# Performance work log

Hardware: AMD Instinct MI355X
Metric: run time of the kernel (lower is better)

Reference implementation:

```python
import jax, jax.numpy as jnp
import numpy as np

B, S, D = 2, 2048, 2048
H, KVH, HD = 32, 8, 64  # n_heads, n_kv_heads, head_dim
REP = H // KVH


def setup_inputs() -> dict:
    key = jax.random.key(0)
    k0, k1, k2, k3, k4 = jax.random.split(key, 5)
    x = jax.random.normal(k0, (B, S, D), dtype=jnp.float32)
    # Linear weights stored as (in, out); matches torch nn.Linear(in,out).weight.T
    scale = 1.0 / np.sqrt(D)
    wq = jax.random.normal(k1, (D, H * HD), dtype=jnp.float32) * scale
    wk = jax.random.normal(k2, (D, KVH * HD), dtype=jnp.float32) * scale
    wv = jax.random.normal(k3, (D, KVH * HD), dtype=jnp.float32) * scale
    wo = jax.random.normal(k4, (H * HD, D), dtype=jnp.float32) * scale
    mask = jnp.tril(jnp.ones((S, S), dtype=bool))[None, None]  # [1,1,S,S] causal
    return {"x": x, "wq": wq, "wk": wk, "wv": wv, "wo": wo, "mask": mask}


def reference(x, wq, wk, wv, wo, mask):
    # Projections
    q = (x @ wq).reshape(B, S, KVH, REP, HD)   # Q head h = g*REP + r -> group g
    k = (x @ wk).reshape(B, S, KVH, HD)
    v = (x @ wv).reshape(B, S, KVH, HD)
    # Grouped attention: never materialize repeated K/V (same math as repeat_kv)
    scores = jnp.einsum('bqgrd,bkgd->bgrqk', q, k) / jnp.sqrt(jnp.asarray(HD, x.dtype))
    m = mask[:, :, None]  # [1,1,1,S,S] broadcasts over (group, rep)
    scores = jnp.where(m, scores, -jnp.inf)
    probs = jax.nn.softmax(scores, axis=-1)  # [B,KVH,REP,S,S]
    out = jnp.einsum('bgrqk,bkgd->bqgrd', probs, v)  # [B,S,KVH,REP,HD]
    out = out.reshape(B, S, H * HD)
    return out @ wo
```

## Files before the change

kernel.cpp:

```cpp
#include <hip/hip_runtime.h>
#include <stdint.h>

typedef __bf16 bf16x8 __attribute__((ext_vector_type(8)));
typedef float  f32x4  __attribute__((ext_vector_type(4)));
typedef float  f32x16 __attribute__((ext_vector_type(16)));

#define QSCALE 0.18033688011112042f

typedef __attribute__((address_space(1))) const void* as1cv;
typedef __attribute__((address_space(3))) void*       as3v;

__device__ __forceinline__ void gload16(const void* g, void* l) {
  __builtin_amdgcn_global_load_lds((as1cv)g, (as3v)l, 16, 0, 0);
}

__device__ __forceinline__ unsigned short f2b(float f) {
  union { float f; unsigned int u; } v; v.f = f;
  unsigned int r = v.u + 0x7fffu + ((v.u >> 16) & 1u);
  return (unsigned short)(r >> 16);
}

__device__ __forceinline__ float b2f(unsigned short s) {
  union { unsigned int u; float f; } v; v.u = (unsigned int)s << 16;
  return v.f;
}

#if __has_builtin(__builtin_amdgcn_exp2f)
__device__ __forceinline__ float fexp2(float x) { return __builtin_amdgcn_exp2f(x); }
#else
__device__ __forceinline__ float fexp2(float x) {
  float r;
  asm volatile("v_exp_f32 %0, %1\n\ts_nop 1" : "=v"(r) : "v"(x));
  return r;
}
#endif

__global__ void detect_dtype(const unsigned short* __restrict__ x, int* __restrict__ flag) {
  const int t = threadIdx.x;
  bool big = false;
  for (int i = t; i < 1024; i += 64) {
    float f = b2f(x[i]);
    if (!(fabsf(f) < 1e6f)) big = true;
  }
  if (t == 0) *flag = 0;
  __syncthreads();
  if (__any(big) && t == 0) *flag = 1;
}

__global__ __launch_bounds__(256) void convert_x(const void* __restrict__ src,
                                                 unsigned short* __restrict__ dst,
                                                 const int* __restrict__ flag) {
  const int i = blockIdx.x * 256 + threadIdx.x;
  if (*flag) {
    float4 a = ((const float4*)src)[2 * i];
    float4 b = ((const float4*)src)[2 * i + 1];
    union { unsigned short o[8]; uint4 v; } u;
    u.o[0] = f2b(a.x); u.o[1] = f2b(a.y); u.o[2] = f2b(a.z); u.o[3] = f2b(a.w);
    u.o[4] = f2b(b.x); u.o[5] = f2b(b.y); u.o[6] = f2b(b.z); u.o[7] = f2b(b.w);
    ((uint4*)dst)[i] = u.v;
  } else {
    ((uint4*)dst)[i] = ((const uint4*)src)[i];
  }
}

__global__ __launch_bounds__(256) void transpose_w(const void* __restrict__ src, int R, int C,
                                                   unsigned short* __restrict__ dst,
                                                   const int* __restrict__ flag) {
  __shared__ unsigned short tile[64][72];
  const int t = threadIdx.x;
  const int r = t >> 2;
  const int c0 = (t & 3) << 4;
  const int gr = blockIdx.y * 64 + r;
  const int gc = blockIdx.x * 64 + c0;
  if (*flag) {
    const float* s = (const float*)src + (size_t)gr * C + gc;
#pragma unroll
    for (int j = 0; j < 16; j += 4) {
      float4 v = *(const float4*)(s + j);
      tile[r][c0 + j + 0] = f2b(v.x);
      tile[r][c0 + j + 1] = f2b(v.y);
      tile[r][c0 + j + 2] = f2b(v.z);
      tile[r][c0 + j + 3] = f2b(v.w);
    }
  } else {
    const unsigned short* s = (const unsigned short*)src + (size_t)gr * C + gc;
    *(uint4*)&tile[r][c0]     = *(const uint4*)s;
    *(uint4*)&tile[r][c0 + 8] = *(const uint4*)(s + 8);
  }
  __syncthreads();
  const int c    = t >> 2;
  const int rblk = (t & 3) << 4;
  union { unsigned short o[16]; uint4 v[2]; } u;
#pragma unroll
  for (int j = 0; j < 16; ++j) u.o[j] = tile[rblk + j][c];
  unsigned short* d = dst + (size_t)(blockIdx.x * 64 + c) * R + blockIdx.y * 64 + rblk;
  *(uint4*)d       = u.v[0];
  *(uint4*)(d + 8) = u.v[1];
}

__global__ __launch_bounds__(256) void gemm_bt2(const unsigned short* __restrict__ A,
                                                const unsigned short* __restrict__ Bt,
                                                void* __restrict__ Cv,
                                                unsigned short* __restrict__ vtout,
                                                int M, int N, int K, int scale_cols,
                                                const int* __restrict__ f32flag) {
  __shared__ unsigned short As[2][128 * 64];
  __shared__ unsigned short Bs[2][128 * 64];
  const int t = threadIdx.x;
  const int lane = t & 63;
  const int wave = t >> 6;
  const int wm = wave >> 1, wn = wave & 1;
  int bx, by;
  {
    const int nx = (int)gridDim.x;
    const int nwg = nx * (int)gridDim.y;
    const int wg = (int)blockIdx.y * nx + (int)blockIdx.x;
    const int cpx = nwg >> 3;
    const int swz = (wg & 7) * cpx + (wg >> 3);
    bx = swz % nx; by = swz / nx;
  }
  const int m0 = by * 128, n0 = bx * 128;
  const int fr = lane & 15;
  const int kb = (lane >> 4) << 4;

  int rowS[4], dofS[4], scS[4];
#pragma unroll
  for (int i = 0; i < 4; ++i) {
    int off = i * 4096 + t * 16;
    dofS[i] = off;
    rowS[i] = off >> 7;
    scS[i]  = (off & 127) ^ ((rowS[i] & 7) << 4);
  }
  const char* pA[4];
  const char* pB[4];
#pragma unroll
  for (int i = 0; i < 4; ++i) {
    pA[i] = (const char*)(A  + (size_t)(m0 + rowS[i]) * K) + scS[i];
    pB[i] = (const char*)(Bt + (size_t)(n0 + rowS[i]) * K) + scS[i];
  }

  f32x4 acc[4][4] = {};
  const int NT = K >> 6;

#pragma unroll
  for (int i = 0; i < 4; ++i) {
    gload16(pA[i], (char*)As[0] + dofS[i]);
    gload16(pB[i], (char*)Bs[0] + dofS[i]);
  }
  __syncthreads();

  for (int kt = 0; kt < NT; ++kt) {
    if (kt + 1 < NT) {
      const int kby = (kt + 1) * 128;
      const int bsel = (kt + 1) & 1;
#pragma unroll
      for (int i = 0; i < 4; ++i) {
        gload16(pA[i] + kby, (char*)As[bsel] + dofS[i]);
        gload16(pB[i] + kby, (char*)Bs[bsel] + dofS[i]);
      }
    }
    const char* Ab = (const char*)As[kt & 1];
    const char* Bb = (const char*)Bs[kt & 1];
#pragma unroll
    for (int ks = 0; ks < 2; ++ks) {
      bf16x8 af[4], bfv[4];
#pragma unroll
      for (int i = 0; i < 4; ++i) {
        const int ra = wm * 64 + i * 16 + fr;
        af[i] = *(const bf16x8*)(Ab + ra * 128 + ((ks * 64 + kb) ^ ((ra & 7) << 4)));
        const int rb = wn * 64 + i * 16 + fr;
        bfv[i] = *(const bf16x8*)(Bb + rb * 128 + ((ks * 64 + kb) ^ ((rb & 7) << 4)));
      }
      __builtin_amdgcn_s_setprio(1);
#pragma unroll
      for (int i = 0; i < 4; ++i)
#pragma unroll
        for (int j = 0; j < 4; ++j)
          acc[i][j] = __builtin_amdgcn_mfma_f32_16x16x32_bf16(af[i], bfv[j], acc[i][j], 0, 0, 0);
      __builtin_amdgcn_s_setprio(0);
    }
    __syncthreads();
  }

  const int cm0 = m0 + wm * 64 + ((lane >> 4) << 2);
  const int cn0 = n0 + wn * 64 + fr;
  if (vtout && n0 >= 2560) {
    const int bb = m0 >> 11;
#pragma unroll
    for (int i = 0; i < 4; ++i) {
      const int s0 = cm0 + i * 16;
#pragma unroll
      for (int j = 0; j < 4; ++j) {
        const int d = cn0 + j * 16 - 2560;
        uint2 pr;
        pr.x = (unsigned int)f2b(acc[i][j][0]) | ((unsigned int)f2b(acc[i][j][1]) << 16);
        pr.y = (unsigned int)f2b(acc[i][j][2]) | ((unsigned int)f2b(acc[i][j][3]) << 16);
        *(uint2*)(vtout + (size_t)(bb * 512 + d) * 2048 + (s0 & 2047)) = pr;
      }
    }
    return;
  }
  const bool of32 = f32flag && (*f32flag != 0);
  if (of32) {
    float* C = (float*)Cv;
#pragma unroll
    for (int i = 0; i < 4; ++i)
#pragma unroll
      for (int j = 0; j < 4; ++j) {
        float sc = (cn0 + j * 16 < scale_cols) ? QSCALE : 1.0f;
#pragma unroll
        for (int r = 0; r < 4; ++r)
          C[(size_t)(cm0 + i * 16 + r) * N + (cn0 + j * 16)] = acc[i][j][r] * sc;
      }
  } else {
    unsigned short* C = (unsigned short*)Cv;
#pragma unroll
    for (int i = 0; i < 4; ++i)
#pragma unroll
      for (int j = 0; j < 4; ++j) {
        float sc = (cn0 + j * 16 < scale_cols) ? QSCALE : 1.0f;
#pragma unroll
        for (int r = 0; r < 4; ++r)
          C[(size_t)(cm0 + i * 16 + r) * N + (cn0 + j * 16)] = f2b(acc[i][j][r] * sc);
      }
  }
}

__global__ __launch_bounds__(256) void attn_fwd6(const unsigned short* __restrict__ qkv,
                                                 const unsigned short* __restrict__ vt,
                                                 unsigned short* __restrict__ ob) {
  __shared__ unsigned short Ks[2][64 * 64];
  __shared__ unsigned short Vs[2][64 * 64];
  const int t = threadIdx.x, lane = t & 63, w = t >> 6;
  const int half = lane >> 5, q32 = lane & 31;
  const int g = blockIdx.y, b = blockIdx.z;
  const int h = g * 4 + w;
  const size_t bS = (size_t)b * 2048;
  const size_t vtb = ((size_t)((b << 3) + g)) * 64;

  int rowS[2], dofS[2], cbS[2];
#pragma unroll
  for (int i = 0; i < 2; ++i) {
    int off = i * 4096 + t * 16;
    dofS[i] = off;
    rowS[i] = off >> 7;
    cbS[i]  = (off & 127) ^ ((rowS[i] & 7) << 4);
  }

  for (int ph = 0; ph < 2; ++ph) {
    const int qt32 = ph ? 63 - (int)blockIdx.x : (int)blockIdx.x;
    const int nkt = (qt32 >> 1) + 1;
    const int q_glob = qt32 * 32 + q32;
    if (ph) __syncthreads();

    bf16x8 qf[4];
    {
      const unsigned short* qrow = qkv + (bS + q_glob) * 3072 + h * 64 + half * 8;
#pragma unroll
      for (int c = 0; c < 4; ++c) qf[c] = *(const bf16x8*)(qrow + 16 * c);
    }
    const unsigned short* kp[2];
    const unsigned short* vp[2];
#pragma unroll
    for (int i = 0; i < 2; ++i) {
      kp[i] = qkv + (bS + rowS[i]) * 3072 + 2048 + g * 64 + (cbS[i] >> 1);
      vp[i] = vt + (vtb + rowS[i]) * 2048 + (cbS[i] >> 1);
    }
    f32x16 Ot0 = {}, Ot1 = {};
    float m_run = -1e30f, l_run = 0.f;

#pragma unroll
    for (int i = 0; i < 2; ++i) {
      gload16(kp[i], (char*)Ks[0] + dofS[i]);
      gload16(vp[i], (char*)Vs[0] + dofS[i]);
      kp[i] += 64 * 3072;
      vp[i] += 64;
    }
    int cur = 0;
    for (int kt = 0; kt < nkt; ++kt) {
      __syncthreads();
      if (kt + 1 < nkt) {
#pragma unroll
        for (int i = 0; i < 2; ++i) {
          gload16(kp[i], (char*)Ks[cur ^ 1] + dofS[i]);
          gload16(vp[i], (char*)Vs[cur ^ 1] + dofS[i]);
          kp[i] += 64 * 3072;
          vp[i] += 64;
        }
      }
      const char* Kb = (const char*)Ks[cur];
      const char* Vb = (const char*)Vs[cur];
      const int sk0 = 2 * kt, sk1 = 2 * kt + 1;
      const bool do1 = (sk1 <= qt32);

      f32x16 s0 = {}, s1 = {};
      {
        const int kr0 = q32;
        const int ksw0 = (kr0 & 7) << 4;
        bf16x8 ka0 = *(const bf16x8*)(Kb + kr0 * 128 + ((16 * half) ^ ksw0));
        bf16x8 ka1 = *(const bf16x8*)(Kb + kr0 * 128 + ((32 + 16 * half) ^ ksw0));
        bf16x8 ka2 = *(const bf16x8*)(Kb + kr0 * 128 + ((64 + 16 * half) ^ ksw0));
        bf16x8 ka3 = *(const bf16x8*)(Kb + kr0 * 128 + ((96 + 16 * half) ^ ksw0));
        __builtin_amdgcn_s_setprio(1);
        s0 = __builtin_amdgcn_mfma_f32_32x32x16_bf16(ka0, qf[0], s0, 0, 0, 0);
        s0 = __builtin_amdgcn_mfma_f32_32x32x16_bf16(ka1, qf[1], s0, 0, 0, 0);
        s0 = __builtin_amdgcn_mfma_f32_32x32x16_bf16(ka2, qf[2], s0, 0, 0, 0);
        s0 = __builtin_amdgcn_mfma_f32_32x32x16_bf16(ka3, qf[3], s0, 0, 0, 0);
        __builtin_amdgcn_s_setprio(0);
      }
      if (do1) {
        const int kr1 = 32 + q32;
        const int ksw1 = (kr1 & 7) << 4;
        bf16x8 kb0 = *(const bf16x8*)(Kb + kr1 * 128 + ((16 * half) ^ ksw1));
        bf16x8 kb1 = *(const bf16x8*)(Kb + kr1 * 128 + ((32 + 16 * half) ^ ksw1));
        bf16x8 kb2 = *(const bf16x8*)(Kb + kr1 * 128 + ((64 + 16 * half) ^ ksw1));
        bf16x8 kb3 = *(const bf16x8*)(Kb + kr1 * 128 + ((96 + 16 * half) ^ ksw1));
        __builtin_amdgcn_s_setprio(1);
        s1 = __builtin_amdgcn_mfma_f32_32x32x16_bf16(kb0, qf[0], s1, 0, 0, 0);
        s1 = __builtin_amdgcn_mfma_f32_32x32x16_bf16(kb1, qf[1], s1, 0, 0, 0);
        s1 = __builtin_amdgcn_mfma_f32_32x32x16_bf16(kb2, qf[2], s1, 0, 0, 0);
        s1 = __builtin_amdgcn_mfma_f32_32x32x16_bf16(kb3, qf[3], s1, 0, 0, 0);
        __builtin_amdgcn_s_setprio(0);
      }
      const int qrel = q32 - 4 * half;
      if (sk0 == qt32) {
#pragma unroll
        for (int r = 0; r < 16; ++r) {
          const int pat = (r & 3) + 8 * (r >> 2);
          if (pat > qrel) s0[r] = -1e30f;
        }
      }
      if (do1 && sk1 == qt32) {
#pragma unroll
        for (int r = 0; r < 16; ++r) {
          const int pat = (r & 3) + 8 * (r >> 2);
          if (pat > qrel) s1[r] = -1e30f;
        }
      }
      float pm = s0[0];
#pragma unroll
      for (int r = 1; r < 16; ++r) pm = fmaxf(pm, s0[r]);
      if (do1) {
#pragma unroll
        for (int r = 0; r < 16; ++r) pm = fmaxf(pm, s1[r]);
      }
      pm = fmaxf(pm, __shfl_xor(pm, 32, 64));
      if (!__all(pm - m_run <= 8.f)) {
        const float mn = fmaxf(m_run, pm);
        const float corr = fexp2(m_run - mn);
        m_run = mn;
        l_run *= corr;
#pragma unroll
        for (int r = 0; r < 16; ++r) { Ot0[r] *= corr; Ot1[r] *= corr; }
      }
      float rs = 0.f;
#pragma unroll
      for (int r = 0; r < 16; ++r) { float p = fexp2(s0[r] - m_run); s0[r] = p; rs += p; }
      if (do1) {
#pragma unroll
        for (int r = 0; r < 16; ++r) { float p = fexp2(s1[r] - m_run); s1[r] = p; rs += p; }
      }
      rs += __shfl_xor(rs, 32, 64);
      l_run += rs;
      bf16x8 pf0, pf1, pf2, pf3;
      {
        unsigned int a01, a23, a45, a67;
        asm("v_cvt_pk_bf16_f32 %0, %1, %2" : "=v"(a01) : "v"(s0[0]), "v"(s0[1]));
        asm("v_cvt_pk_bf16_f32 %0, %1, %2" : "=v"(a23) : "v"(s0[2]), "v"(s0[3]));
        asm("v_cvt_pk_bf16_f32 %0, %1, %2" : "=v"(a45) : "v"(s0[4]), "v"(s0[5]));
        asm("v_cvt_pk_bf16_f32 %0, %1, %2" : "=v"(a67) : "v"(s0[6]), "v"(s0[7]));
        asm("v_permlane32_swap_b32 %0, %1" : "+v"(a01), "+v"(a45));
        asm("v_permlane32_swap_b32 %0, %1" : "+v"(a23), "+v"(a67));
        union { unsigned int u[4]; bf16x8 v; } fu;
        fu.u[0] = a01; fu.u[1] = a23; fu.u[2] = a45; fu.u[3] = a67;
        pf0 = fu.v;
        asm("v_cvt_pk_bf16_f32 %0, %1, %2" : "=v"(a01) : "v"(s0[8]),  "v"(s0[9]));
        asm("v_cvt_pk_bf16_f32 %0, %1, %2" : "=v"(a23) : "v"(s0[10]), "v"(s0[11]));
        asm("v_cvt_pk_bf16_f32 %0, %1, %2" : "=v"(a45) : "v"(s0[12]), "v"(s0[13]));
        asm("v_cvt_pk_bf16_f32 %0, %1, %2" : "=v"(a67) : "v"(s0[14]), "v"(s0[15]));
        asm("v_permlane32_swap_b32 %0, %1" : "+v"(a01), "+v"(a45));
        asm("v_permlane32_swap_b32 %0, %1" : "+v"(a23), "+v"(a67));
        fu.u[0] = a01; fu.u[1] = a23; fu.u[2] = a45; fu.u[3] = a67;
        pf1 = fu.v;
      }
      if (do1) {
        unsigned int a01, a23, a45, a67;
        asm("v_cvt_pk_bf16_f32 %0, %1, %2" : "=v"(a01) : "v"(s1[0]), "v"(s1[1]));
        asm("v_cvt_pk_bf16_f32 %0, %1, %2" : "=v"(a23) : "v"(s1[2]), "v"(s1[3]));
        asm("v_cvt_pk_bf16_f32 %0, %1, %2" : "=v"(a45) : "v"(s1[4]), "v"(s1[5]));
        asm("v_cvt_pk_bf16_f32 %0, %1, %2" : "=v"(a67) : "v"(s1[6]), "v"(s1[7]));
        asm("v_permlane32_swap_b32 %0, %1" : "+v"(a01), "+v"(a45));
        asm("v_permlane32_swap_b32 %0, %1" : "+v"(a23), "+v"(a67));
        union { unsigned int u[4]; bf16x8 v; } fu;
        fu.u[0] = a01; fu.u[1] = a23; fu.u[2] = a45; fu.u[3] = a67;
        pf2 = fu.v;
        asm("v_cvt_pk_bf16_f32 %0, %1, %2" : "=v"(a01) : "v"(s1[8]),  "v"(s1[9]));
        asm("v_cvt_pk_bf16_f32 %0, %1, %2" : "=v"(a23) : "v"(s1[10]), "v"(s1[11]));
        asm("v_cvt_pk_bf16_f32 %0, %1, %2" : "=v"(a45) : "v"(s1[12]), "v"(s1[13]));
        asm("v_cvt_pk_bf16_f32 %0, %1, %2" : "=v"(a67) : "v"(s1[14]), "v"(s1[15]));
        asm("v_permlane32_swap_b32 %0, %1" : "+v"(a01), "+v"(a45));
        asm("v_permlane32_swap_b32 %0, %1" : "+v"(a23), "+v"(a67));
        fu.u[0] = a01; fu.u[1] = a23; fu.u[2] = a45; fu.u[3] = a67;
        pf3 = fu.v;
      }
      const int vsw0 = (q32 & 7) << 4;
      {
        const int cbase = 16 * half;
        bf16x8 vf00 = *(const bf16x8*)(Vb + q32 * 128 + (cbase ^ vsw0));
        bf16x8 vf01 = *(const bf16x8*)(Vb + q32 * 128 + ((cbase + 32) ^ vsw0));
        bf16x8 vf10 = *(const bf16x8*)(Vb + (32 + q32) * 128 + (cbase ^ vsw0));
        bf16x8 vf11 = *(const bf16x8*)(Vb + (32 + q32) * 128 + ((cbase + 32) ^ vsw0));
        __builtin_amdgcn_s_setprio(1);
        Ot0 = __builtin_amdgcn_mfma_f32_32x32x16_bf16(vf00, pf0, Ot0, 0, 0, 0);
        Ot0 = __builtin_amdgcn_mfma_f32_32x32x16_bf16(vf01, pf1, Ot0, 0, 0, 0);
        Ot1 = __builtin_amdgcn_mfma_f32_32x32x16_bf16(vf10, pf0, Ot1, 0, 0, 0);
        Ot1 = __builtin_amdgcn_mfma_f32_32x32x16_bf16(vf11, pf1, Ot1, 0, 0, 0);
        __builtin_amdgcn_s_setprio(0);
      }
      if (do1) {
        const int cbase = 64 + 16 * half;
        bf16x8 vf00 = *(const bf16x8*)(Vb + q32 * 128 + (cbase ^ vsw0));
        bf16x8 vf01 = *(const bf16x8*)(Vb + q32 * 128 + ((cbase + 32) ^ vsw0));
        bf16x8 vf10 = *(const bf16x8*)(Vb + (32 + q32) * 128 + (cbase ^ vsw0));
        bf16x8 vf11 = *(const bf16x8*)(Vb + (32 + q32) * 128 + ((cbase + 32) ^ vsw0));
        __builtin_amdgcn_s_setprio(1);
        Ot0 = __builtin_amdgcn_mfma_f32_32x32x16_bf16(vf00, pf2, Ot0, 0, 0, 0);
        Ot0 = __builtin_amdgcn_mfma_f32_32x32x16_bf16(vf01, pf3, Ot0, 0, 0, 0);
        Ot1 = __builtin_amdgcn_mfma_f32_32x32x16_bf16(vf10, pf2, Ot1, 0, 0, 0);
        Ot1 = __builtin_amdgcn_mfma_f32_32x32x16_bf16(vf11, pf3, Ot1, 0, 0, 0);
        __builtin_amdgcn_s_setprio(0);
      }
      cur ^= 1;
    }
    const float inv = 1.f / l_run;
    unsigned short* orow = ob + (bS + q_glob) * 2048 + h * 64;
#pragma unroll
    for (int j = 0; j < 4; ++j) {
      uint2 pr;
      pr.x = (unsigned int)f2b(Ot0[4 * j + 0] * inv) | ((unsigned int)f2b(Ot0[4 * j + 1] * inv) << 16);
      pr.y = (unsigned int)f2b(Ot0[4 * j + 2] * inv) | ((unsigned int)f2b(Ot0[4 * j + 3] * inv) << 16);
      *(uint2*)(orow + 8 * j + 4 * half) = pr;
      uint2 pr2;
      pr2.x = (unsigned int)f2b(Ot1[4 * j + 0] * inv) | ((unsigned int)f2b(Ot1[4 * j + 1] * inv) << 16);
      pr2.y = (unsigned int)f2b(Ot1[4 * j + 2] * inv) | ((unsigned int)f2b(Ot1[4 * j + 3] * inv) << 16);
      *(uint2*)(orow + 32 + 8 * j + 4 * half) = pr2;
    }
  }
}

extern "C" void kernel_launch(void* const* d_in, const int* in_sizes, int n_in,
                              void* d_out, int out_size, void* d_ws, size_t ws_size,
                              hipStream_t stream) {
  (void)in_sizes; (void)n_in; (void)out_size; (void)ws_size;
  const void* x  = d_in[0];
  const void* wq = d_in[1];
  const void* wk = d_in[2];
  const void* wv = d_in[3];
  const void* wo = d_in[4];
  unsigned short* ws = (unsigned short*)d_ws;

  int* FLAG = (int*)ws;
  unsigned short* WT  = ws + 128;
  unsigned short* WOT = WT  + (size_t)3072 * 2048;
  unsigned short* QKV = WOT + (size_t)2048 * 2048;
  unsigned short* VT  = QKV + (size_t)4096 * 3072;
  unsigned short* OB  = VT  + (size_t)16 * 64 * 2048;
  unsigned short* XB  = OB;

  detect_dtype<<<1, 64, 0, stream>>>((const unsigned short*)x, FLAG);

  transpose_w<<<dim3(32, 32), 256, 0, stream>>>(wq, 2048, 2048, WT, FLAG);
  transpose_w<<<dim3(8, 32), 256, 0, stream>>>(wk, 2048, 512, WT + (size_t)2048 * 2048, FLAG);
  transpose_w<<<dim3(8, 32), 256, 0, stream>>>(wv, 2048, 512, WT + (size_t)2560 * 2048, FLAG);
  transpose_w<<<dim3(32, 32), 256, 0, stream>>>(wo, 2048, 2048, WOT, FLAG);
  convert_x<<<4096, 256, 0, stream>>>(x, XB, FLAG);

  gemm_bt2<<<dim3(24, 32), 256, 0, stream>>>(XB, WT, QKV, VT, 4096, 3072, 2048, 2048, nullptr);
  attn_fwd6<<<dim3(32, 8, 2), 256, 0, stream>>>(QKV, VT, OB);
  gemm_bt2<<<dim3(16, 32), 256, 0, stream>>>(OB, WOT, d_out, nullptr, 4096, 2048, 2048, 0, FLAG);
}
```

Baseline: 195.8 us.

## Split paired causal q-tiles into separate blocks with heavy-first 1D scheduling

The attention kernel previously processed two complementary q-tiles per block (a light one, then a heavy one) to balance causal work. It now launches one block per q-tile over a flat 1024-block grid, ordered so the longest tiles are dispatched first, and adds a min-blocks-per-CU launch bound of 4. The row max and row sum reductions are rewritten as trees to shorten dependency chains. The intent is better load balancing and occupancy at the cost of twice as many blocks, repeated Q setup, and possible register pressure from the launch bound.

```diff
diff --git a/kernel.cpp b/kernel.cpp
--- a/kernel.cpp
+++ b/kernel.cpp
@@ -226,17 +226,24 @@
   }
 }
 
-__global__ __launch_bounds__(256) void attn_fwd6(const unsigned short* __restrict__ qkv,
-                                                 const unsigned short* __restrict__ vt,
-                                                 unsigned short* __restrict__ ob) {
+__global__ __launch_bounds__(256, 4) void attn_fwd7(const unsigned short* __restrict__ qkv,
+                                                    const unsigned short* __restrict__ vt,
+                                                    unsigned short* __restrict__ ob) {
   __shared__ unsigned short Ks[2][64 * 64];
   __shared__ unsigned short Vs[2][64 * 64];
   const int t = threadIdx.x, lane = t & 63, w = t >> 6;
   const int half = lane >> 5, q32 = lane & 31;
-  const int g = blockIdx.y, b = blockIdx.z;
+  const int lin = (int)blockIdx.x;
+  const int rr = lin >> 8;
+  const int k  = (lin & 255) >> 4;
+  const int gb = lin & 15;
+  const int g = gb & 7, b = gb >> 3;
+  const int qt = (rr == 0) ? 63 - k : (rr == 1) ? 32 + k : (rr == 2) ? 31 - k : k;
   const int h = g * 4 + w;
   const size_t bS = (size_t)b * 2048;
   const size_t vtb = ((size_t)((b << 3) + g)) * 64;
+  const int nkt = (qt >> 1) + 1;
+  const int q_glob = qt * 32 + q32;
 
   int rowS[2], dofS[2], cbS[2];
 #pragma unroll
@@ -247,204 +254,209 @@
     cbS[i]  = (off & 127) ^ ((rowS[i] & 7) << 4);
   }
 
-  for (int ph = 0; ph < 2; ++ph) {
-    const int qt32 = ph ? 63 - (int)blockIdx.x : (int)blockIdx.x;
-    const int nkt = (qt32 >> 1) + 1;
-    const int q_glob = qt32 * 32 + q32;
-    if (ph) __syncthreads();
-
-    bf16x8 qf[4];
+  bf16x8 qf[4];
+  {
+    const unsigned short* qrow = qkv + (bS + q_glob) * 3072 + h * 64 + half * 8;
+#pragma unroll
+    for (int c = 0; c < 4; ++c) qf[c] = *(const bf16x8*)(qrow + 16 * c);
+  }
+  const unsigned short* kp[2];
+  const unsigned short* vp[2];
+#pragma unroll
+  for (int i = 0; i < 2; ++i) {
+    kp[i] = qkv + (bS + rowS[i]) * 3072 + 2048 + g * 64 + (cbS[i] >> 1);
+    vp[i] = vt + (vtb + rowS[i]) * 2048 + (cbS[i] >> 1);
+  }
+  f32x16 Ot0 = {}, Ot1 = {};
+  float m_run = -1e30f, l_run = 0.f;
+
+#pragma unroll
+  for (int i = 0; i < 2; ++i) {
+    gload16(kp[i], (char*)Ks[0] + dofS[i]);
+    gload16(vp[i], (char*)Vs[0] + dofS[i]);
+    kp[i] += 64 * 3072;
+    vp[i] += 64;
+  }
+  int cur = 0;
+  for (int kt = 0; kt < nkt; ++kt) {
+    __syncthreads();
+    if (kt + 1 < nkt) {
+#pragma unroll
+      for (int i = 0; i < 2; ++i) {
+        gload16(kp[i], (char*)Ks[cur ^ 1] + dofS[i]);
+        gload16(vp[i], (char*)Vs[cur ^ 1] + dofS[i]);
+        kp[i] += 64 * 3072;
+        vp[i] += 64;
+      }
+    }
+    const char* Kb = (const char*)Ks[cur];
+    const char* Vb = (const char*)Vs[cur];
+    const int sk0 = 2 * kt, sk1 = 2 * kt + 1;
+    const bool do1 = (sk1 <= qt);
+
+    f32x16 s0 = {}, s1 = {};
     {
-      const unsigned short* qrow = qkv + (bS + q_glob) * 3072 + h * 64 + half * 8;
-#pragma unroll
-      for (int c = 0; c < 4; ++c) qf[c] = *(const bf16x8*)(qrow + 16 * c);
-    }
-    const unsigned short* kp[2];
-    const unsigned short* vp[2];
-#pragma unroll
-    for (int i = 0; i < 2; ++i) {
-      kp[i] = qkv + (bS + rowS[i]) * 3072 + 2048 + g * 64 + (cbS[i] >> 1);
-      vp[i] = vt + (vtb + rowS[i]) * 2048 + (cbS[i] >> 1);
-    }
-    f32x16 Ot0 = {}, Ot1 = {};
-    float m_run = -1e30f, l_run = 0.f;
-
-#pragma unroll
-    for (int i = 0; i < 2; ++i) {
-      gload16(kp[i], (char*)Ks[0] + dofS[i]);
-      gload16(vp[i], (char*)Vs[0] + dofS[i]);
-      kp[i] += 64 * 3072;
-      vp[i] += 64;
-    }
-    int cur = 0;
-    for (int kt = 0; kt < nkt; ++kt) {
-      __syncthreads();
-      if (kt + 1 < nkt) {
-#pragma unroll
-        for (int i = 0; i < 2; ++i) {
-          gload16(kp[i], (char*)Ks[cur ^ 1] + dofS[i]);
-          gload16(vp[i], (char*)Vs[cur ^ 1] + dofS[i]);
-          kp[i] += 64 * 3072;
-          vp[i] += 64;
-        }
-      }
-      const char* Kb = (const char*)Ks[cur];
-      const char* Vb = (const char*)Vs[cur];
-      const int sk0 = 2 * kt, sk1 = 2 * kt + 1;
-      const bool do1 = (sk1 <= qt32);
-
-      f32x16 s0 = {}, s1 = {};
-      {
-        const int kr0 = q32;
-        const int ksw0 = (kr0 & 7) << 4;
-        bf16x8 ka0 = *(const bf16x8*)(Kb + kr0 * 128 + ((16 * half) ^ ksw0));
-        bf16x8 ka1 = *(const bf16x8*)(Kb + kr0 * 128 + ((32 + 16 * half) ^ ksw0));
-        bf16x8 ka2 = *(const bf16x8*)(Kb + kr0 * 128 + ((64 + 16 * half) ^ ksw0));
-        bf16x8 ka3 = *(const bf16x8*)(Kb + kr0 * 128 + ((96 + 16 * half) ^ ksw0));
-        __builtin_amdgcn_s_setprio(1);
-        s0 = __builtin_amdgcn_mfma_f32_32x32x16_bf16(ka0, qf[0], s0, 0, 0, 0);
-        s0 = __builtin_amdgcn_mfma_f32_32x32x16_bf16(ka1, qf[1], s0, 0, 0, 0);
-        s0 = __builtin_amdgcn_mfma_f32_32x32x16_bf16(ka2, qf[2], s0, 0, 0, 0);
-        s0 = __builtin_amdgcn_mfma_f32_32x32x16_bf16(ka3, qf[3], s0, 0, 0, 0);
-        __builtin_amdgcn_s_setprio(0);
-      }
-      if (do1) {
-        const int kr1 = 32 + q32;
-        const int ksw1 = (kr1 & 7) << 4;
-        bf16x8 kb0 = *(const bf16x8*)(Kb + kr1 * 128 + ((16 * half) ^ ksw1));
-        bf16x8 kb1 = *(const bf16x8*)(Kb + kr1 * 128 + ((32 + 16 * half) ^ ksw1));
-        bf16x8 kb2 = *(const bf16x8*)(Kb + kr1 * 128 + ((64 + 16 * half) ^ ksw1));
-        bf16x8 kb3 = *(const bf16x8*)(Kb + kr1 * 128 + ((96 + 16 * half) ^ ksw1));
-        __builtin_amdgcn_s_setprio(1);
-        s1 = __builtin_amdgcn_mfma_f32_32x32x16_bf16(kb0, qf[0], s1, 0, 0, 0);
-        s1 = __builtin_amdgcn_mfma_f32_32x32x16_bf16(kb1, qf[1], s1, 0, 0, 0);
-        s1 = __builtin_amdgcn_mfma_f32_32x32x16_bf16(kb2, qf[2], s1, 0, 0, 0);
-        s1 = __builtin_amdgcn_mfma_f32_32x32x16_bf16(kb3, qf[3], s1, 0, 0, 0);
-        __builtin_amdgcn_s_setprio(0);
-      }
-      const int qrel = q32 - 4 * half;
-      if (sk0 == qt32) {
-#pragma unroll
-        for (int r = 0; r < 16; ++r) {
-          const int pat = (r & 3) + 8 * (r >> 2);
-          if (pat > qrel) s0[r] = -1e30f;
-        }
-      }
-      if (do1 && sk1 == qt32) {
-#pragma unroll
-        for (int r = 0; r < 16; ++r) {
-          const int pat = (r & 3) + 8 * (r >> 2);
-          if (pat > qrel) s1[r] = -1e30f;
-        }
-      }
-      float pm = s0[0];
-#pragma unroll
-      for (int r = 1; r < 16; ++r) pm = fmaxf(pm, s0[r]);
-      if (do1) {
-#pragma unroll
-        for (int r = 0; r < 16; ++r) pm = fmaxf(pm, s1[r]);
-      }
-      pm = fmaxf(pm, __shfl_xor(pm, 32, 64));
-      if (!__all(pm - m_run <= 8.f)) {
-        const float mn = fmaxf(m_run, pm);
-        const float corr = fexp2(m_run - mn);
-        m_run = mn;
-        l_run *= corr;
-#pragma unroll
-        for (int r = 0; r < 16; ++r) { Ot0[r] *= corr; Ot1[r] *= corr; }
-      }
-      float rs = 0.f;
-#pragma unroll
-      for (int r = 0; r < 16; ++r) { float p = fexp2(s0[r] - m_run); s0[r] = p; rs += p; }
-      if (do1) {
-#pragma unroll
-        for (int r = 0; r < 16; ++r) { float p = fexp2(s1[r] - m_run); s1[r] = p; rs += p; }
-      }
-      rs += __shfl_xor(rs, 32, 64);
-      l_run += rs;
-      bf16x8 pf0, pf1, pf2, pf3;
-      {
-        unsigned int a01, a23, a45, a67;
-        asm("v_cvt_pk_bf16_f32 %0, %1, %2" : "=v"(a01) : "v"(s0[0]), "v"(s0[1]));
-        asm("v_cvt_pk_bf16_f32 %0, %1, %2" : "=v"(a23) : "v"(s0[2]), "v"(s0[3]));
-        asm("v_cvt_pk_bf16_f32 %0, %1, %2" : "=v"(a45) : "v"(s0[4]), "v"(s0[5]));
-        asm("v_cvt_pk_bf16_f32 %0, %1, %2" : "=v"(a67) : "v"(s0[6]), "v"(s0[7]));
-        asm("v_permlane32_swap_b32 %0, %1" : "+v"(a01), "+v"(a45));
-        asm("v_permlane32_swap_b32 %0, %1" : "+v"(a23), "+v"(a67));
-        union { unsigned int u[4]; bf16x8 v; } fu;
-        fu.u[0] = a01; fu.u[1] = a23; fu.u[2] = a45; fu.u[3] = a67;
-        pf0 = fu.v;
-        asm("v_cvt_pk_bf16_f32 %0, %1, %2" : "=v"(a01) : "v"(s0[8]),  "v"(s0[9]));
-        asm("v_cvt_pk_bf16_f32 %0, %1, %2" : "=v"(a23) : "v"(s0[10]), "v"(s0[11]));
-        asm("v_cvt_pk_bf16_f32 %0, %1, %2" : "=v"(a45) : "v"(s0[12]), "v"(s0[13]));
-        asm("v_cvt_pk_bf16_f32 %0, %1, %2" : "=v"(a67) : "v"(s0[14]), "v"(s0[15]));
-        asm("v_permlane32_swap_b32 %0, %1" : "+v"(a01), "+v"(a45));
-        asm("v_permlane32_swap_b32 %0, %1" : "+v"(a23), "+v"(a67));
-        fu.u[0] = a01; fu.u[1] = a23; fu.u[2] = a45; fu.u[3] = a67;
-        pf1 = fu.v;
-      }
-      if (do1) {
-        unsigned int a01, a23, a45, a67;
-        asm("v_cvt_pk_bf16_f32 %0, %1, %2" : "=v"(a01) : "v"(s1[0]), "v"(s1[1]));
-        asm("v_cvt_pk_bf16_f32 %0, %1, %2" : "=v"(a23) : "v"(s1[2]), "v"(s1[3]));
-        asm("v_cvt_pk_bf16_f32 %0, %1, %2" : "=v"(a45) : "v"(s1[4]), "v"(s1[5]));
-        asm("v_cvt_pk_bf16_f32 %0, %1, %2" : "=v"(a67) : "v"(s1[6]), "v"(s1[7]));
-        asm("v_permlane32_swap_b32 %0, %1" : "+v"(a01), "+v"(a45));
-        asm("v_permlane32_swap_b32 %0, %1" : "+v"(a23), "+v"(a67));
-        union { unsigned int u[4]; bf16x8 v; } fu;
-        fu.u[0] = a01; fu.u[1] = a23; fu.u[2] = a45; fu.u[3] = a67;
-        pf2 = fu.v;
-        asm("v_cvt_pk_bf16_f32 %0, %1, %2" : "=v"(a01) : "v"(s1[8]),  "v"(s1[9]));
-        asm("v_cvt_pk_bf16_f32 %0, %1, %2" : "=v"(a23) : "v"(s1[10]), "v"(s1[11]));
-        asm("v_cvt_pk_bf16_f32 %0, %1, %2" : "=v"(a45) : "v"(s1[12]), "v"(s1[13]));
-        asm("v_cvt_pk_bf16_f32 %0, %1, %2" : "=v"(a67) : "v"(s1[14]), "v"(s1[15]));
-        asm("v_permlane32_swap_b32 %0, %1" : "+v"(a01), "+v"(a45));
-        asm("v_permlane32_swap_b32 %0, %1" : "+v"(a23), "+v"(a67));
-        fu.u[0] = a01; fu.u[1] = a23; fu.u[2] = a45; fu.u[3] = a67;
-        pf3 = fu.v;
-      }
-      const int vsw0 = (q32 & 7) << 4;
-      {
-        const int cbase = 16 * half;
-        bf16x8 vf00 = *(const bf16x8*)(Vb + q32 * 128 + (cbase ^ vsw0));
-        bf16x8 vf01 = *(const bf16x8*)(Vb + q32 * 128 + ((cbase + 32) ^ vsw0));
-        bf16x8 vf10 = *(const bf16x8*)(Vb + (32 + q32) * 128 + (cbase ^ vsw0));
-        bf16x8 vf11 = *(const bf16x8*)(Vb + (32 + q32) * 128 + ((cbase + 32) ^ vsw0));
-        __builtin_amdgcn_s_setprio(1);
-        Ot0 = __builtin_amdgcn_mfma_f32_32x32x16_bf16(vf00, pf0, Ot0, 0, 0, 0);
-        Ot0 = __builtin_amdgcn_mfma_f32_32x32x16_bf16(vf01, pf1, Ot0, 0, 0, 0);
-        Ot1 = __builtin_amdgcn_mfma_f32_32x32x16_bf16(vf10, pf0, Ot1, 0, 0, 0);
-        Ot1 = __builtin_amdgcn_mfma_f32_32x32x16_bf16(vf11, pf1, Ot1, 0, 0, 0);
-        __builtin_amdgcn_s_setprio(0);
-      }
-      if (do1) {
-        const int cbase = 64 + 16 * half;
-        bf16x8 vf00 = *(const bf16x8*)(Vb + q32 * 128 + (cbase ^ vsw0));
-        bf16x8 vf01 = *(const bf16x8*)(Vb + q32 * 128 + ((cbase + 32) ^ vsw0));
-        bf16x8 vf10 = *(const bf16x8*)(Vb + (32 + q32) * 128 + (cbase ^ vsw0));
-        bf16x8 vf11 = *(const bf16x8*)(Vb + (32 + q32) * 128 + ((cbase + 32) ^ vsw0));
-        __builtin_amdgcn_s_setprio(1);
-        Ot0 = __builtin_amdgcn_mfma_f32_32x32x16_bf16(vf00, pf2, Ot0, 0, 0, 0);
-        Ot0 = __builtin_amdgcn_mfma_f32_32x32x16_bf16(vf01, pf3, Ot0, 0, 0, 0);
-        Ot1 = __builtin_amdgcn_mfma_f32_32x32x16_bf16(vf10, pf2, Ot1, 0, 0, 0);
-        Ot1 = __builtin_amdgcn_mfma_f32_32x32x16_bf16(vf11, pf3, Ot1, 0, 0, 0);
-        __builtin_amdgcn_s_setprio(0);
-      }
-      cur ^= 1;
-    }
-    const float inv = 1.f / l_run;
-    unsigned short* orow = ob + (bS + q_glob) * 2048 + h * 64;
-#pragma unroll
-    for (int j = 0; j < 4; ++j) {
-      uint2 pr;
-      pr.x = (unsigned int)f2b(Ot0[4 * j + 0] * inv) | ((unsigned int)f2b(Ot0[4 * j + 1] * inv) << 16);
-      pr.y = (unsigned int)f2b(Ot0[4 * j + 2] * inv) | ((unsigned int)f2b(Ot0[4 * j + 3] * inv) << 16);
-      *(uint2*)(orow + 8 * j + 4 * half) = pr;
-      uint2 pr2;
-      pr2.x = (unsigned int)f2b(Ot1[4 * j + 0] * inv) | ((unsigned int)f2b(Ot1[4 * j + 1] * inv) << 16);
-      pr2.y = (unsigned int)f2b(Ot1[4 * j + 2] * inv) | ((unsigned int)f2b(Ot1[4 * j + 3] * inv) << 16);
-      *(uint2*)(orow + 32 + 8 * j + 4 * half) = pr2;
-    }
+      const int kr0 = q32;
+      const int ksw0 = (kr0 & 7) << 4;
+      bf16x8 ka0 = *(const bf16x8*)(Kb + kr0 * 128 + ((16 * half) ^ ksw0));
+      bf16x8 ka1 = *(const bf16x8*)(Kb + kr0 * 128 + ((32 + 16 * half) ^ ksw0));
+      bf16x8 ka2 = *(const bf16x8*)(Kb + kr0 * 128 + ((64 + 16 * half) ^ ksw0));
+      bf16x8 ka3 = *(const bf16x8*)(Kb + kr0 * 128 + ((96 + 16 * half) ^ ksw0));
+      __builtin_amdgcn_s_setprio(1);
+      s0 = __builtin_amdgcn_mfma_f32_32x32x16_bf16(ka0, qf[0], s0, 0, 0, 0);
+      s0 = __builtin_amdgcn_mfma_f32_32x32x16_bf16(ka1, qf[1], s0, 0, 0, 0);
+      s0 = __builtin_amdgcn_mfma_f32_32x32x16_bf16(ka2, qf[2], s0, 0, 0, 0);
+      s0 = __builtin_amdgcn_mfma_f32_32x32x16_bf16(ka3, qf[3], s0, 0, 0, 0);
+      __builtin_amdgcn_s_setprio(0);
+    }
+    if (do1) {
+      const int kr1 = 32 + q32;
+      const int ksw1 = (kr1 & 7) << 4;
+      bf16x8 kb0 = *(const bf16x8*)(Kb + kr1 * 128 + ((16 * half) ^ ksw1));
+      bf16x8 kb1 = *(const bf16x8*)(Kb + kr1 * 128 + ((32 + 16 * half) ^ ksw1));
+      bf16x8 kb2 = *(const bf16x8*)(Kb + kr1 * 128 + ((64 + 16 * half) ^ ksw1));
+      bf16x8 kb3 = *(const bf16x8*)(Kb + kr1 * 128 + ((96 + 16 * half) ^ ksw1));
+      __builtin_amdgcn_s_setprio(1);
+      s1 = __builtin_amdgcn_mfma_f32_32x32x16_bf16(kb0, qf[0], s1, 0, 0, 0);
+      s1 = __builtin_amdgcn_mfma_f32_32x32x16_bf16(kb1, qf[1], s1, 0, 0, 0);
+      s1 = __builtin_amdgcn_mfma_f32_32x32x16_bf16(kb2, qf[2], s1, 0, 0, 0);
+      s1 = __builtin_amdgcn_mfma_f32_32x32x16_bf16(kb3, qf[3], s1, 0, 0, 0);
+      __builtin_amdgcn_s_setprio(0);
+    }
+    const int qrel = q32 - 4 * half;
+    if (sk0 == qt) {
+#pragma unroll
+      for (int r = 0; r < 16; ++r) {
+        const int pat = (r & 3) + 8 * (r >> 2);
+        if (pat > qrel) s0[r] = -1e30f;
+      }
+    }
+    if (do1 && sk1 == qt) {
+#pragma unroll
+      for (int r = 0; r < 16; ++r) {
+        const int pat = (r & 3) + 8 * (r >> 2);
+        if (pat > qrel) s1[r] = -1e30f;
+      }
+    }
+    float tm[8];
+#pragma unroll
+    for (int r = 0; r < 8; ++r) tm[r] = fmaxf(s0[r], s0[r + 8]);
+    if (do1) {
+#pragma unroll
+      for (int r = 0; r < 8; ++r) tm[r] = fmaxf(tm[r], fmaxf(s1[r], s1[r + 8]));
+    }
+#pragma unroll
+    for (int r = 0; r < 4; ++r) tm[r] = fmaxf(tm[r], tm[r + 4]);
+    float pm = fmaxf(fmaxf(tm[0], tm[1]), fmaxf(tm[2], tm[3]));
+    pm = fmaxf(pm, __shfl_xor(pm, 32, 64));
+    if (!__all(pm - m_run <= 8.f)) {
+      const float mn = fmaxf(m_run, pm);
+      const float corr = fexp2(m_run - mn);
+      m_run = mn;
+      l_run *= corr;
+#pragma unroll
+      for (int r = 0; r < 16; ++r) { Ot0[r] *= corr; Ot1[r] *= corr; }
+    }
+    float ts[8];
+#pragma unroll
+    for (int r = 0; r < 16; ++r) s0[r] = fexp2(s0[r] - m_run);
+    if (do1) {
+#pragma unroll
+      for (int r = 0; r < 16; ++r) s1[r] = fexp2(s1[r] - m_run);
+    }
+#pragma unroll
+    for (int r = 0; r < 8; ++r) ts[r] = s0[r] + s0[r + 8];
+    if (do1) {
+#pragma unroll
+      for (int r = 0; r < 8; ++r) ts[r] += s1[r] + s1[r + 8];
+    }
+#pragma unroll
+    for (int r = 0; r < 4; ++r) ts[r] += ts[r + 4];
+    float rs = (ts[0] + ts[1]) + (ts[2] + ts[3]);
+    rs += __shfl_xor(rs, 32, 64);
+    l_run += rs;
+    bf16x8 pf0, pf1, pf2, pf3;
+    {
+      unsigned int a01, a23, a45, a67;
+      asm("v_cvt_pk_bf16_f32 %0, %1, %2" : "=v"(a01) : "v"(s0[0]), "v"(s0[1]));
+      asm("v_cvt_pk_bf16_f32 %0, %1, %2" : "=v"(a23) : "v"(s0[2]), "v"(s0[3]));
+      asm("v_cvt_pk_bf16_f32 %0, %1, %2" : "=v"(a45) : "v"(s0[4]), "v"(s0[5]));
+      asm("v_cvt_pk_bf16_f32 %0, %1, %2" : "=v"(a67) : "v"(s0[6]), "v"(s0[7]));
+      asm("v_permlane32_swap_b32 %0, %1" : "+v"(a01), "+v"(a45));
+      asm("v_permlane32_swap_b32 %0, %1" : "+v"(a23), "+v"(a67));
+      union { unsigned int u[4]; bf16x8 v; } fu;
+      fu.u[0] = a01; fu.u[1] = a23; fu.u[2] = a45; fu.u[3] = a67;
+      pf0 = fu.v;
+      asm("v_cvt_pk_bf16_f32 %0, %1, %2" : "=v"(a01) : "v"(s0[8]),  "v"(s0[9]));
+      asm("v_cvt_pk_bf16_f32 %0, %1, %2" : "=v"(a23) : "v"(s0[10]), "v"(s0[11]));
+      asm("v_cvt_pk_bf16_f32 %0, %1, %2" : "=v"(a45) : "v"(s0[12]), "v"(s0[13]));
+      asm("v_cvt_pk_bf16_f32 %0, %1, %2" : "=v"(a67) : "v"(s0[14]), "v"(s0[15]));
+      asm("v_permlane32_swap_b32 %0, %1" : "+v"(a01), "+v"(a45));
+      asm("v_permlane32_swap_b32 %0, %1" : "+v"(a23), "+v"(a67));
+      fu.u[0] = a01; fu.u[1] = a23; fu.u[2] = a45; fu.u[3] = a67;
+      pf1 = fu.v;
+    }
+    if (do1) {
+      unsigned int a01, a23, a45, a67;
+      asm("v_cvt_pk_bf16_f32 %0, %1, %2" : "=v"(a01) : "v"(s1[0]), "v"(s1[1]));
+      asm("v_cvt_pk_bf16_f32 %0, %1, %2" : "=v"(a23) : "v"(s1[2]), "v"(s1[3]));
+      asm("v_cvt_pk_bf16_f32 %0, %1, %2" : "=v"(a45) : "v"(s1[4]), "v"(s1[5]));
+      asm("v_cvt_pk_bf16_f32 %0, %1, %2" : "=v"(a67) : "v"(s1[6]), "v"(s1[7]));
+      asm("v_permlane32_swap_b32 %0, %1" : "+v"(a01), "+v"(a45));
+      asm("v_permlane32_swap_b32 %0, %1" : "+v"(a23), "+v"(a67));
+      union { unsigned int u[4]; bf16x8 v; } fu;
+      fu.u[0] = a01; fu.u[1] = a23; fu.u[2] = a45; fu.u[3] = a67;
+      pf2 = fu.v;
+      asm("v_cvt_pk_bf16_f32 %0, %1, %2" : "=v"(a01) : "v"(s1[8]),  "v"(s1[9]));
+      asm("v_cvt_pk_bf16_f32 %0, %1, %2" : "=v"(a23) : "v"(s1[10]), "v"(s1[11]));
+      asm("v_cvt_pk_bf16_f32 %0, %1, %2" : "=v"(a45) : "v"(s1[12]), "v"(s1[13]));
+      asm("v_cvt_pk_bf16_f32 %0, %1, %2" : "=v"(a67) : "v"(s1[14]), "v"(s1[15]));
+      asm("v_permlane32_swap_b32 %0, %1" : "+v"(a01), "+v"(a45));
+      asm("v_permlane32_swap_b32 %0, %1" : "+v"(a23), "+v"(a67));
+      fu.u[0] = a01; fu.u[1] = a23; fu.u[2] = a45; fu.u[3] = a67;
+      pf3 = fu.v;
+    }
+    const int vsw0 = (q32 & 7) << 4;
+    {
+      const int cbase = 16 * half;
+      bf16x8 vf00 = *(const bf16x8*)(Vb + q32 * 128 + (cbase ^ vsw0));
+      bf16x8 vf01 = *(const bf16x8*)(Vb + q32 * 128 + ((cbase + 32) ^ vsw0));
+      bf16x8 vf10 = *(const bf16x8*)(Vb + (32 + q32) * 128 + (cbase ^ vsw0));
+      bf16x8 vf11 = *(const bf16x8*)(Vb + (32 + q32) * 128 + ((cbase + 32) ^ vsw0));
+      __builtin_amdgcn_s_setprio(1);
+      Ot0 = __builtin_amdgcn_mfma_f32_32x32x16_bf16(vf00, pf0, Ot0, 0, 0, 0);
+      Ot0 = __builtin_amdgcn_mfma_f32_32x32x16_bf16(vf01, pf1, Ot0, 0, 0, 0);
+      Ot1 = __builtin_amdgcn_mfma_f32_32x32x16_bf16(vf10, pf0, Ot1, 0, 0, 0);
+      Ot1 = __builtin_amdgcn_mfma_f32_32x32x16_bf16(vf11, pf1, Ot1, 0, 0, 0);
+      __builtin_amdgcn_s_setprio(0);
+    }
+    if (do1) {
+      const int cbase = 64 + 16 * half;
+      bf16x8 vf00 = *(const bf16x8*)(Vb + q32 * 128 + (cbase ^ vsw0));
+      bf16x8 vf01 = *(const bf16x8*)(Vb + q32 * 128 + ((cbase + 32) ^ vsw0));
+      bf16x8 vf10 = *(const bf16x8*)(Vb + (32 + q32) * 128 + (cbase ^ vsw0));
+      bf16x8 vf11 = *(const bf16x8*)(Vb + (32 + q32) * 128 + ((cbase + 32) ^ vsw0));
+      __builtin_amdgcn_s_setprio(1);
+      Ot0 = __builtin_amdgcn_mfma_f32_32x32x16_bf16(vf00, pf2, Ot0, 0, 0, 0);
+      Ot0 = __builtin_amdgcn_mfma_f32_32x32x16_bf16(vf01, pf3, Ot0, 0, 0, 0);
+      Ot1 = __builtin_amdgcn_mfma_f32_32x32x16_bf16(vf10, pf2, Ot1, 0, 0, 0);
+      Ot1 = __builtin_amdgcn_mfma_f32_32x32x16_bf16(vf11, pf3, Ot1, 0, 0, 0);
+      __builtin_amdgcn_s_setprio(0);
+    }
+    cur ^= 1;
+  }
+  const float inv = 1.f / l_run;
+  unsigned short* orow = ob + (bS + q_glob) * 2048 + h * 64;
+#pragma unroll
+  for (int j = 0; j < 4; ++j) {
+    uint2 pr;
+    pr.x = (unsigned int)f2b(Ot0[4 * j + 0] * inv) | ((unsigned int)f2b(Ot0[4 * j + 1] * inv) << 16);
+    pr.y = (unsigned int)f2b(Ot0[4 * j + 2] * inv) | ((unsigned int)f2b(Ot0[4 * j + 3] * inv) << 16);
+    *(uint2*)(orow + 8 * j + 4 * half) = pr;
+    uint2 pr2;
+    pr2.x = (unsigned int)f2b(Ot1[4 * j + 0] * inv) | ((unsigned int)f2b(Ot1[4 * j + 1] * inv) << 16);
+    pr2.y = (unsigned int)f2b(Ot1[4 * j + 2] * inv) | ((unsigned int)f2b(Ot1[4 * j + 3] * inv) << 16);
+    *(uint2*)(orow + 32 + 8 * j + 4 * half) = pr2;
   }
 }
 
@@ -476,6 +488,6 @@
   convert_x<<<4096, 256, 0, stream>>>(x, XB, FLAG);
 
   gemm_bt2<<<dim3(24, 32), 256, 0, stream>>>(XB, WT, QKV, VT, 4096, 3072, 2048, 2048, nullptr);
-  attn_fwd6<<<dim3(32, 8, 2), 256, 0, stream>>>(QKV, VT, OB);
+  attn_fwd7<<<dim3(1024), 256, 0, stream>>>(QKV, VT, OB);
   gemm_bt2<<<dim3(16, 32), 256, 0, stream>>>(OB, WOT, d_out, nullptr, 4096, 2048, 2048, 0, FLAG);
 }
```

Measured after the change: 181.0 us. 7.6% less time.
